# Performance work log

Hardware: AMD Instinct MI355X
Metric: run time of the kernel (lower is better)

Reference implementation:

```python
import jax, jax.numpy as jnp
import numpy as np

HEAD_DIM = 64
NUM_HEADS = 32
ROPE_THETA = 10000.0


def _rope_cos_sin(seq_len, dim, theta, dtype):
    inv_freq = 1.0 / (theta ** (jnp.arange(0, dim, 2, dtype=jnp.float32) / dim))
    t = jnp.arange(seq_len, dtype=jnp.float32)
    freqs = jnp.outer(t, inv_freq)  # [T, dim/2]
    return jnp.cos(freqs).astype(dtype), jnp.sin(freqs).astype(dtype)


def _apply_rope(x, cos, sin):
    # x: [B, T, H, D]; GPT-NeoX style (split halves), matching flash-attn rotary (interleaved=False)
    d2 = x.shape[-1] // 2
    x1, x2 = x[..., :d2], x[..., d2:]
    c = cos[None, :, None, :]
    s = sin[None, :, None, :]
    return jnp.concatenate([x1 * c - x2 * s, x2 * c + x1 * s], axis=-1)


def setup_inputs() -> dict:
    key = jax.random.key(0)
    ks = jax.random.split(key, 8)
    B, T, Dm = 2, 2048, 2048
    H, Dh = NUM_HEADS, HEAD_DIM
    sc = 1.0 / np.sqrt(Dm)
    return {
        "hidden_states": jax.random.normal(ks[0], (B, T, Dm), jnp.float32),
        "v1": jax.random.normal(ks[1], (B, T, H, Dh), jnp.float32),
        "lambda1": jax.random.uniform(ks[2], (), jnp.float32),
        "Wq": jax.random.normal(ks[3], (Dm, Dm), jnp.float32) * sc,
        "Wk": jax.random.normal(ks[4], (Dm, Dm), jnp.float32) * sc,
        "Wv": jax.random.normal(ks[5], (Dm, Dm), jnp.float32) * sc,
        "Wo": jax.random.normal(ks[6], (Dm, Dm), jnp.float32) * sc,
        "lambda2": jnp.float32(0.5),
    }


def reference(hidden_states, v1, lambda1, Wq, Wk, Wv, Wo, lambda2):
    B, T, Dm = hidden_states.shape
    H, Dh = NUM_HEADS, HEAD_DIM
    # QKV projections + head split
    q = (hidden_states @ Wq).reshape(B, T, H, Dh)
    k = (hidden_states @ Wk).reshape(B, T, H, Dh)
    v = (hidden_states @ Wv).reshape(B, T, H, Dh)
    # Value residual mixing: V' = lambda1 * V_1 + lambda2 * V_n
    v = lambda1 * v1 + lambda2 * v
    # RoPE (seqlen_offset = 0, no cache)
    cos, sin = _rope_cos_sin(T, Dh, ROPE_THETA, q.dtype)
    q = _apply_rope(q, cos, sin)
    k = _apply_rope(k, cos, sin)
    # Causal attention (flash_attn_func(..., causal=True) equivalent)
    scale = 1.0 / np.sqrt(Dh)
    scores = jnp.einsum("bqhd,bkhd->bhqk", q, k) * scale
    causal = jnp.tril(jnp.ones((T, T), dtype=bool))
    scores = jnp.where(causal[None, None], scores, jnp.finfo(scores.dtype).min)
    probs = jax.nn.softmax(scores, axis=-1)
    o = jnp.einsum("bhqk,bkhd->bqhd", probs, v).reshape(B, T, Dm)
    return o @ Wo
```

## Files before the change

kernel.cpp:

```cpp
#include <hip/hip_runtime.h>
#include <hip/hip_bf16.h>
#include <math.h>

typedef __bf16 bf16;
typedef __bf16 bf16x8 __attribute__((ext_vector_type(8)));
typedef __bf16 bf16x4 __attribute__((ext_vector_type(4)));
typedef float  f32x4  __attribute__((ext_vector_type(4)));
typedef short  sv4    __attribute__((ext_vector_type(4)));

#define B_  2
#define T_  2048
#define DM  2048
#define H_  32
#define DH  64

__device__ __forceinline__ bf16x8 load8(const bf16* p) {
    return *reinterpret_cast<const bf16x8*>(p);
}

__device__ __forceinline__ void gld16(const bf16* g, bf16* l) {
    __builtin_amdgcn_global_load_lds(
        (const __attribute__((address_space(1))) unsigned int*)g,
        (__attribute__((address_space(3))) unsigned int*)l, 16, 0, 0);
}

__global__ void k_convert(const float* __restrict__ in, bf16* __restrict__ out, int n4) {
    int i = blockIdx.x * blockDim.x + threadIdx.x;
    if (i < n4) {
        float4 v = reinterpret_cast<const float4*>(in)[i];
        bf16x4 o;
        o[0] = (bf16)v.x; o[1] = (bf16)v.y; o[2] = (bf16)v.z; o[3] = (bf16)v.w;
        reinterpret_cast<bf16x4*>(out)[i] = o;
    }
}

__global__ void k_transposeW(const float* __restrict__ Wq, const float* __restrict__ Wk,
                             const float* __restrict__ Wv, const float* __restrict__ Wo,
                             bf16* __restrict__ WqT, bf16* __restrict__ WkT,
                             bf16* __restrict__ WvT, bf16* __restrict__ WoT) {
    const float* in; bf16* out;
    switch (blockIdx.z) {
        case 0: in = Wq; out = WqT; break;
        case 1: in = Wk; out = WkT; break;
        case 2: in = Wv; out = WvT; break;
        default: in = Wo; out = WoT; break;
    }
    __shared__ float tile[32][33];
    int tx = threadIdx.x, ty = threadIdx.y;
    int x0 = blockIdx.x * 32, y0 = blockIdx.y * 32;
    #pragma unroll
    for (int i = 0; i < 4; i++)
        tile[ty + i*8][tx] = in[(size_t)(y0 + ty + i*8) * DM + x0 + tx];
    __syncthreads();
    #pragma unroll
    for (int i = 0; i < 4; i++)
        out[(size_t)(x0 + ty + i*8) * DM + y0 + tx] = (bf16)tile[tx][ty + i*8];
}

template<int OUT_BF16>
__global__ __launch_bounds__(256)
void k_gemm(const bf16* __restrict__ A, const bf16* __restrict__ BT,
            void* __restrict__ Cout, int ldc) {
    constexpr int K = 2048;
    __shared__ bf16 ldsA[128 * 32];
    __shared__ bf16 ldsB[128 * 32];
    int tid = threadIdx.x;
    int lane = tid & 63, w = tid >> 6;
    int l16 = lane & 15, quad = lane >> 4;
    int wm = w >> 1, wn = w & 1;
    int mblk = blockIdx.y * 128, nblk = blockIdx.x * 128;

    f32x4 acc[4][4] = {};

    int sgz = ((lane & 3) ^ ((lane >> 3) & 3)) * 8;
    const bf16* gA = A  + (size_t)(mblk + w * 32 + (lane >> 2)) * K + sgz;
    const bf16* gB = BT + (size_t)(nblk + w * 32 + (lane >> 2)) * K + sgz;
    bf16* lA = ldsA + w * 1024;
    bf16* lB = ldsB + w * 1024;
    int sA = (quad ^ ((l16 >> 1) & 3)) * 8;

    for (int k0 = 0; k0 < K; k0 += 32) {
        gld16(gA + k0,          lA);
        gld16(gA + 16 * K + k0, lA + 512);
        gld16(gB + k0,          lB);
        gld16(gB + 16 * K + k0, lB + 512);
        __syncthreads();
        bf16x8 af[4], bfr[4];
        #pragma unroll
        for (int s = 0; s < 4; s++)
            af[s] = *reinterpret_cast<bf16x8*>(&ldsA[(wm * 64 + s * 16 + l16) * 32 + sA]);
        #pragma unroll
        for (int t = 0; t < 4; t++)
            bfr[t] = *reinterpret_cast<bf16x8*>(&ldsB[(wn * 64 + t * 16 + l16) * 32 + sA]);
        #pragma unroll
        for (int s = 0; s < 4; s++)
            #pragma unroll
            for (int t = 0; t < 4; t++)
                acc[s][t] = __builtin_amdgcn_mfma_f32_16x16x32_bf16(af[s], bfr[t], acc[s][t], 0, 0, 0);
        __syncthreads();
    }

    #pragma unroll
    for (int s = 0; s < 4; s++) {
        int row = mblk + wm * 64 + s * 16 + quad * 4;
        #pragma unroll
        for (int t = 0; t < 4; t++) {
            int col = nblk + wn * 64 + t * 16 + l16;
            #pragma unroll
            for (int r = 0; r < 4; r++) {
                if (OUT_BF16)
                    reinterpret_cast<bf16*>(Cout)[(size_t)(row + r) * ldc + col] = (bf16)acc[s][t][r];
                else
                    reinterpret_cast<float*>(Cout)[(size_t)(row + r) * ldc + col] = acc[s][t][r];
            }
        }
    }
}

template<int OUT_BF16>
__global__ __launch_bounds__(512, 2)
void k_gemm256(const bf16* __restrict__ A, const bf16* __restrict__ BT,
               void* __restrict__ Cout, int ldc) {
    constexpr int K = 2048;
    extern __shared__ bf16 lds[];
    const int tid  = threadIdx.x;
    const int lane = tid & 63, w = tid >> 6;
    const int l16  = lane & 15, quad = lane >> 4;
    const int wm   = w >> 2, wn = w & 3;
    const size_t mblk = (size_t)blockIdx.y * 256, nblk = (size_t)blockIdx.x * 256;

    f32x4 acc[8][4] = {};

    const int sg = (((tid & 3) ^ ((tid >> 3) & 3)) << 3);
    const bf16* gA = A  + (mblk + (tid >> 2)) * K + sg;
    const bf16* gB = BT + (nblk + (tid >> 2)) * K + sg;

    const int segr = ((quad ^ ((l16 >> 1) & 3)) << 3);
    const int aoff = (wm * 128 + l16) * 32 + segr;
    const int boff = (wn * 64  + l16) * 32 + segr;

#define STG(kt_, buf_) do { \
    const bf16* ga_ = gA + (kt_) * 32; \
    const bf16* gb_ = gB + (kt_) * 32; \
    bf16* lb_ = lds + (buf_) * 16384 + w * 512; \
    bf16* la_ = lds + (buf_) * 16384 + 8192 + w * 512; \
    gld16(gb_, lb_); gld16(gb_ + 128 * 2048, lb_ + 4096); \
    gld16(ga_, la_); gld16(ga_ + 128 * 2048, la_ + 4096); \
} while (0)

#define BAR  __builtin_amdgcn_s_barrier()
#define PRI1 __builtin_amdgcn_s_setprio(1)
#define PRI0 __builtin_amdgcn_s_setprio(0)
#define VM4  asm volatile("s_waitcnt vmcnt(4)" ::: "memory")
#define VM0  asm volatile("s_waitcnt vmcnt(0)" ::: "memory")

#define TILE(cb_, SG_, VM_) do { \
    const bf16* rb_ = lds + (cb_) + boff; \
    const bf16* ra_ = lds + (cb_) + 8192 + aoff; \
    bf16x8 af[8], bq[4]; \
    _Pragma("unroll") for (int i_ = 0; i_ < 8; ++i_) \
        af[i_] = *reinterpret_cast<const bf16x8*>(ra_ + i_ * 512); \
    _Pragma("unroll") for (int i_ = 0; i_ < 4; ++i_) \
        bq[i_] = *reinterpret_cast<const bf16x8*>(rb_ + i_ * 512); \
    SG_; \
    VM_; \
    BAR; \
    PRI1; \
    _Pragma("unroll") for (int mi_ = 0; mi_ < 8; ++mi_) \
        _Pragma("unroll") for (int ni_ = 0; ni_ < 4; ++ni_) \
            acc[mi_][ni_] = __builtin_amdgcn_mfma_f32_16x16x32_bf16( \
                af[mi_], bq[ni_], acc[mi_][ni_], 0, 0, 0); \
    PRI0; \
} while (0)

    STG(0, 0); STG(1, 1);
    VM4;
    BAR;

    #pragma unroll 1
    for (int t = 0; t < 60; t += 3) {
        TILE(0,     STG(t + 2, 2), VM4);
        TILE(16384, STG(t + 3, 0), VM4);
        TILE(32768, STG(t + 4, 1), VM4);
    }
    TILE(0,     STG(62, 2), VM4);
    TILE(16384, STG(63, 0), VM4);
    TILE(32768, (void)0,    VM0);
    TILE(0,     (void)0,    (void)0);

#undef STG
#undef BAR
#undef PRI1
#undef PRI0
#undef VM4
#undef VM0
#undef TILE

    #pragma unroll
    for (int mt = 0; mt < 8; ++mt) {
        size_t row = mblk + wm * 128 + mt * 16 + quad * 4;
        #pragma unroll
        for (int nt = 0; nt < 4; ++nt) {
            size_t col = nblk + wn * 64 + nt * 16 + l16;
            #pragma unroll
            for (int r = 0; r < 4; ++r) {
                if (OUT_BF16)
                    reinterpret_cast<bf16*>(Cout)[(row + r) * (size_t)ldc + col] = (bf16)acc[mt][nt][r];
                else
                    reinterpret_cast<float*>(Cout)[(row + r) * (size_t)ldc + col] = acc[mt][nt][r];
            }
        }
    }
}

namespace {
struct GemmLdsInit {
    GemmLdsInit() {
        (void)hipFuncSetAttribute(
            reinterpret_cast<const void*>(&k_gemm256<1>),
            hipFuncAttributeMaxDynamicSharedMemorySize, 98304);
    }
};
GemmLdsInit g_ldsInit;
}

__global__ void k_tab(float2* __restrict__ tab) {
    int id = blockIdx.x * 256 + threadIdx.x;
    int i = id & 31, t = id >> 5;
    float inv = __builtin_amdgcn_exp2f(-(float)i * 0.41524101186092037f);
    float ang = (float)t * inv;
    float s, c;
    __sincosf(ang, &s, &c);
    tab[id] = make_float2(c, s);
}

__global__ void k_rope(bf16* __restrict__ qkv, const float2* __restrict__ tab) {
    int id = blockIdx.x * 256 + threadIdx.x;
    int j   = id & 3;
    int h   = (id >> 2) & 31;
    int sel = (id >> 7) & 1;
    int t   = (id >> 8) & 2047;
    int b   = id >> 19;
    size_t base = ((size_t)(b * T_ + t)) * 6144 + sel * 2048 + h * 64 + j * 8;
    bf16x8 x1 = load8(qkv + base);
    bf16x8 x2 = load8(qkv + base + 32);
    const float2* tp = tab + t * 32 + j * 8;
    bf16x8 o1, o2;
    #pragma unroll
    for (int e = 0; e < 8; e++) {
        float c = tp[e].x, s = tp[e].y;
        float a = (float)x1[e], v = (float)x2[e];
        o1[e] = (bf16)(a * c - v * s);
        o2[e] = (bf16)(v * c + a * s);
    }
    *reinterpret_cast<bf16x8*>(qkv + base)      = o1;
    *reinterpret_cast<bf16x8*>(qkv + base + 32) = o2;
}

__global__ void k_combinev(const float* __restrict__ v1, const bf16* __restrict__ qkv,
                           const float* __restrict__ l1p, const float* __restrict__ l2p,
                           bf16* __restrict__ vT) {
    __shared__ float tile[64 * 33];
    float l1 = l1p[0], l2 = l2p[0];
    int b = blockIdx.y >> 5, h = blockIdx.y & 31;
    int t0 = blockIdx.x * 32;
    int tid = threadIdx.x;
    int d = tid & 63, tr = tid >> 6;
    #pragma unroll
    for (int i = 0; i < 8; i++) {
        int t = t0 + i * 4 + tr;
        size_t iv1 = ((size_t)(b * T_ + t)) * 2048 + h * 64 + d;
        size_t ivg = ((size_t)(b * T_ + t)) * 6144 + 4096 + h * 64 + d;
        tile[d * 33 + i * 4 + tr] = l1 * v1[iv1] + l2 * (float)qkv[ivg];
    }
    __syncthreads();
    int tl = tid & 31, dr = tid >> 5;
    #pragma unroll
    for (int j = 0; j < 8; j++) {
        int d2 = dr + j * 8;
        vT[((size_t)((b * H_ + h) * 64 + d2)) * T_ + t0 + tl] = (bf16)tile[d2 * 33 + tl];
    }
}

__global__ __launch_bounds__(256)
void k_attn(const bf16* __restrict__ qkv, const bf16* __restrict__ vT, bf16* __restrict__ o) {
    __shared__ bf16 ldsK[64 * 64];
    __shared__ bf16 ldsV[64 * 64];
    int bx = blockIdx.x;
    int bh = blockIdx.y;
    int b = bh >> 5, h = bh & 31;
    int tid = threadIdx.x;
    int lane = tid & 63, w = tid >> 6;
    int l16 = lane & 15, quad = lane >> 4;

    int rl = lane >> 3, sg = ((lane & 7) ^ rl) * 8;
    const bf16* kgl = qkv + ((size_t)(b * T_) + w * 16 + rl) * 6144 + 2048 + h * 64 + sg;
    const bf16* vgl = vT + ((size_t)bh * DH + w * 16 + rl) * T_ + sg;
    bf16* lKw = ldsK + w * 16 * 64;
    bf16* lVw = ldsV + w * 16 * 64;

    int skey = (quad ^ (l16 & 7)) * 8;
    int skey2 = ((quad + 4) ^ (l16 & 7)) * 8;

    #pragma unroll 1
    for (int pass = 0; pass < 2; pass++) {
        int qt = pass ? (31 - bx) : bx;
        int qbase = qt * 64 + w * 16;

        size_t qrow = (size_t)(b * T_ + qbase + l16) * 6144 + h * 64;
        bf16x8 qf[2];
        #pragma unroll
        for (int half = 0; half < 2; half++) {
            bf16x8 v = load8(qkv + qrow + half * 32 + quad * 8);
            #pragma unroll
            for (int e = 0; e < 8; e++) v[e] = (bf16)((float)v[e] * 0.1803368801f);
            qf[half] = v;
        }

        f32x4 accO[4] = {};
        float m_ = -1e30f, pl = 0.f;

        int nkt = qt + 1;
        for (int kt = 0; kt < nkt; kt++) {
            int key0 = kt * 64;
            #pragma unroll
            for (int j = 0; j < 2; j++) {
                gld16(kgl + (size_t)(key0 + j * 8) * 6144, lKw + j * 512);
                gld16(vgl + (size_t)(j * 8) * T_ + key0,   lVw + j * 512);
            }
            __syncthreads();

            bool diag = (kt == qt);
            f32x4 st[4];
            sv4 pk[4];
            #pragma unroll
            for (int ks = 0; ks < 4; ks++) {
                if (!diag || key0 + ks * 16 <= qbase + 15) {
                    bf16x8 kf0 = *reinterpret_cast<bf16x8*>(&ldsK[(ks * 16 + l16) * 64 + skey]);
                    bf16x8 kf1 = *reinterpret_cast<bf16x8*>(&ldsK[(ks * 16 + l16) * 64 + skey2]);
                    f32x4 z = {};
                    z = __builtin_amdgcn_mfma_f32_16x16x32_bf16(kf0, qf[0], z, 0, 0, 0);
                    z = __builtin_amdgcn_mfma_f32_16x16x32_bf16(kf1, qf[1], z, 0, 0, 0);
                    st[ks] = z;
                } else {
                    st[ks] = (f32x4){-3e38f, -3e38f, -3e38f, -3e38f};
                }
            }

            if (diag) {
                int qcol = qbase + l16;
                #pragma unroll
                for (int ks = 0; ks < 4; ks++)
                    #pragma unroll
                    for (int r = 0; r < 4; r++)
                        if (key0 + ks * 16 + quad * 4 + r > qcol) st[ks][r] = -3e38f;
            }

            float mx = st[0][0];
            #pragma unroll
            for (int ks = 0; ks < 4; ks++)
                #pragma unroll
                for (int r = 0; r < 4; r++) mx = fmaxf(mx, st[ks][r]);
            mx = fmaxf(mx, __shfl_xor(mx, 16));
            mx = fmaxf(mx, __shfl_xor(mx, 32));
            if (__any(mx > m_)) {
                float nm = fmaxf(m_, mx);
                float alpha = __builtin_amdgcn_exp2f(m_ - nm);
                m_ = nm;
                pl *= alpha;
                #pragma unroll
                for (int n2 = 0; n2 < 4; n2++) accO[n2] *= alpha;
            }
            float rsum = 0.f;
            #pragma unroll
            for (int ks = 0; ks < 4; ks++) {
                bf16x4 ph;
                #pragma unroll
                for (int r = 0; r < 4; r++) {
                    float p = __builtin_amdgcn_exp2f(st[ks][r] - m_);
                    rsum += p;
                    ph[r] = (bf16)p;
                }
                pk[ks] = __builtin_bit_cast(sv4, ph);
            }
            pl += rsum;

            #pragma unroll
            for (int ks = 0; ks < 4; ks++) {
                if (!diag || key0 + ks * 16 <= qbase + 15) {
                    int svf = ((ks * 2 + (quad >> 1)) ^ (l16 & 7)) * 8 + (quad & 1) * 4;
                    #pragma unroll
                    for (int n2 = 0; n2 < 4; n2++) {
                        sv4 vf = *reinterpret_cast<sv4*>(&ldsV[(n2 * 16 + l16) * 64 + svf]);
                        accO[n2] = __builtin_amdgcn_mfma_f32_16x16x16bf16_1k(
                            vf, pk[ks], accO[n2], 0, 0, 0);
                    }
                }
            }
            __syncthreads();
        }

        float l = pl;
        l += __shfl_xor(l, 16);
        l += __shfl_xor(l, 32);
        float inv = 1.0f / l;
        int query = qbase + l16;
        #pragma unroll
        for (int n2 = 0; n2 < 4; n2++) {
            bf16x4 ov;
            #pragma unroll
            for (int r = 0; r < 4; r++) ov[r] = (bf16)(accO[n2][r] * inv);
            *reinterpret_cast<bf16x4*>(
                &o[(size_t)(b * T_ + query) * DM + h * 64 + n2 * 16 + quad * 4]) = ov;
        }
    }
}

extern "C" void kernel_launch(void* const* d_in, const int* in_sizes, int n_in,
                              void* d_out, int out_size, void* d_ws, size_t ws_size,
                              hipStream_t stream) {
    const float* hs   = (const float*)d_in[0];
    const float* v1   = (const float*)d_in[1];
    const float* lam1 = (const float*)d_in[2];
    const float* Wq   = (const float*)d_in[3];
    const float* Wk   = (const float*)d_in[4];
    const float* Wv   = (const float*)d_in[5];
    const float* Wo   = (const float*)d_in[6];
    const float* lam2 = (const float*)d_in[7];

    char* ws = (char*)d_ws;
    bf16* hs_bf = (bf16*)(ws);
    float2* tab = (float2*)(ws);
    bf16* Wcat  = (bf16*)(ws + 16777216);
    bf16* WoT   = (bf16*)(ws + 41943040);
    bf16* qkv   = (bf16*)(ws + 50331648);
    bf16* vT_bf = (bf16*)(ws + 100663296);
    bf16* o_bf  = (bf16*)(ws + 117440512);

    k_convert<<<8192, 256, 0, stream>>>(hs, hs_bf, 2097152);
    k_transposeW<<<dim3(64, 64, 4), dim3(32, 8), 0, stream>>>(
        Wq, Wk, Wv, Wo, Wcat, Wcat + 4194304, Wcat + 8388608, WoT);

    k_gemm256<1><<<dim3(24, 16), 512, 98304, stream>>>(hs_bf, Wcat, (void*)qkv, 6144);

    k_tab<<<256, 256, 0, stream>>>(tab);
    k_rope<<<4096, 256, 0, stream>>>(qkv, tab);

    k_combinev<<<dim3(64, 64), 256, 0, stream>>>(v1, qkv, lam1, lam2, vT_bf);

    k_attn<<<dim3(16, 64), 256, 0, stream>>>(qkv, vT_bf, o_bf);

    k_gemm<0><<<dim3(16, 32), 256, 0, stream>>>(o_bf, WoT, d_out, 2048);
}
```

Baseline: 430.3 us.

## Restructure QKV GEMM with K=64 double-buffered tiles and interleaved MFMA/LDS schedule

The 256x256 QKV GEMM moves from K=32 triple-buffered LDS stages to K=64 double-buffered stages (128 KB LDS). Each tile is split into four MFMA sub-phases with LDS fragment loads and global-to-LDS stages interleaved between barriers, and the LDS swizzle is widened to 8 segments. Block indices are also remapped with a 1D grid so blocks are assigned in an XCD-aware order. This aims to halve barrier and loop overhead per K step and to overlap memory traffic with compute. The cost is more barriers per tile, and the larger LDS footprint likely rules out two blocks per CU.

```diff
diff --git a/kernel.cpp b/kernel.cpp
--- a/kernel.cpp
+++ b/kernel.cpp
@@ -127,71 +127,90 @@
     const int lane = tid & 63, w = tid >> 6;
     const int l16  = lane & 15, quad = lane >> 4;
     const int wm   = w >> 2, wn = w & 3;
-    const size_t mblk = (size_t)blockIdx.y * 256, nblk = (size_t)blockIdx.x * 256;
+    const int nb   = (blockIdx.x & 7) * 48 + (blockIdx.x >> 3);
+    const size_t mblk = (size_t)(nb / 24) * 256, nblk = (size_t)(nb % 24) * 256;
 
     f32x4 acc[8][4] = {};
 
-    const int sg = (((tid & 3) ^ ((tid >> 3) & 3)) << 3);
-    const bf16* gA = A  + (mblk + (tid >> 2)) * K + sg;
-    const bf16* gB = BT + (nblk + (tid >> 2)) * K + sg;
-
-    const int segr = ((quad ^ ((l16 >> 1) & 3)) << 3);
-    const int aoff = (wm * 128 + l16) * 32 + segr;
-    const int boff = (wn * 64  + l16) * 32 + segr;
-
-#define STG(kt_, buf_) do { \
-    const bf16* ga_ = gA + (kt_) * 32; \
-    const bf16* gb_ = gB + (kt_) * 32; \
-    bf16* lb_ = lds + (buf_) * 16384 + w * 512; \
-    bf16* la_ = lds + (buf_) * 16384 + 8192 + w * 512; \
-    gld16(gb_, lb_); gld16(gb_ + 128 * 2048, lb_ + 4096); \
-    gld16(ga_, la_); gld16(ga_ + 128 * 2048, la_ + 4096); \
+    const int lsg = (((tid & 7) ^ ((tid >> 3) & 7)) << 3);
+    const bf16* gA = A  + (mblk + (tid >> 3)) * K + lsg;
+    const bf16* gB = BT + (nblk + (tid >> 3)) * K + lsg;
+    bf16* lw = lds + w * 512;
+
+    const int seg0 = ((quad ^ (l16 & 7)) << 3);
+    const int seg1 = (((4 + quad) ^ (l16 & 7)) << 3);
+
+#define STG(kt_, r_) do { \
+    const bf16* g_ = (((r_) & 2) ? gA : gB) + (size_t)(((r_) & 1) << 7) * K + (kt_) * 64; \
+    bf16* l_ = lw + (((kt_) & 1) << 15) + ((r_) << 13); \
+    gld16(g_, l_); gld16(g_ + (size_t)64 * K, l_ + 4096); \
 } while (0)
 
+#define LDA(cb_, mh_) do { \
+    _Pragma("unroll") for (int i_ = 0; i_ < 4; ++i_) { \
+        int ro_ = (cb_) + 16384 + (wm * 128 + ((mh_) * 4 + i_) * 16 + l16) * 64; \
+        av[i_][0] = *reinterpret_cast<const bf16x8*>(lds + ro_ + seg0); \
+        av[i_][1] = *reinterpret_cast<const bf16x8*>(lds + ro_ + seg1); \
+    } \
+} while (0)
+
+#define LDB(cb_, nh_) do { \
+    _Pragma("unroll") for (int j_ = 0; j_ < 2; ++j_) { \
+        int ni_ = (nh_) * 2 + j_; \
+        int ro_ = (cb_) + (wn * 64 + ni_ * 16 + l16) * 64; \
+        bv[ni_][0] = *reinterpret_cast<const bf16x8*>(lds + ro_ + seg0); \
+        bv[ni_][1] = *reinterpret_cast<const bf16x8*>(lds + ro_ + seg1); \
+    } \
+} while (0)
+
+#define MF(mh_, nh_) do { \
+    __builtin_amdgcn_s_setprio(1); \
+    _Pragma("unroll") for (int i_ = 0; i_ < 4; ++i_) \
+        _Pragma("unroll") for (int j_ = 0; j_ < 2; ++j_) { \
+            int mi_ = (mh_) * 4 + i_, ni_ = (nh_) * 2 + j_; \
+            acc[mi_][ni_] = __builtin_amdgcn_mfma_f32_16x16x32_bf16( \
+                av[i_][0], bv[ni_][0], acc[mi_][ni_], 0, 0, 0); \
+            acc[mi_][ni_] = __builtin_amdgcn_mfma_f32_16x16x32_bf16( \
+                av[i_][1], bv[ni_][1], acc[mi_][ni_], 0, 0, 0); \
+        } \
+    __builtin_amdgcn_s_setprio(0); \
+} while (0)
+
 #define BAR  __builtin_amdgcn_s_barrier()
-#define PRI1 __builtin_amdgcn_s_setprio(1)
-#define PRI0 __builtin_amdgcn_s_setprio(0)
+#define LGK0 asm volatile("s_waitcnt lgkmcnt(0)" ::: "memory")
 #define VM4  asm volatile("s_waitcnt vmcnt(4)" ::: "memory")
 #define VM0  asm volatile("s_waitcnt vmcnt(0)" ::: "memory")
 
-#define TILE(cb_, SG_, VM_) do { \
-    const bf16* rb_ = lds + (cb_) + boff; \
-    const bf16* ra_ = lds + (cb_) + 8192 + aoff; \
-    bf16x8 af[8], bq[4]; \
-    _Pragma("unroll") for (int i_ = 0; i_ < 8; ++i_) \
-        af[i_] = *reinterpret_cast<const bf16x8*>(ra_ + i_ * 512); \
-    _Pragma("unroll") for (int i_ = 0; i_ < 4; ++i_) \
-        bq[i_] = *reinterpret_cast<const bf16x8*>(rb_ + i_ * 512); \
-    SG_; \
-    VM_; \
-    BAR; \
-    PRI1; \
-    _Pragma("unroll") for (int mi_ = 0; mi_ < 8; ++mi_) \
-        _Pragma("unroll") for (int ni_ = 0; ni_ < 4; ++ni_) \
-            acc[mi_][ni_] = __builtin_amdgcn_mfma_f32_16x16x32_bf16( \
-                af[mi_], bq[ni_], acc[mi_][ni_], 0, 0, 0); \
-    PRI0; \
+#define TILE(cb_, S1_, S3_, S4_, VM_) do { \
+    bf16x8 av[4][2], bv[4][2]; \
+    LDA(cb_, 0); LDB(cb_, 0); \
+    S1_; BAR; LGK0; MF(0, 0); BAR; \
+    LDB(cb_, 1); \
+    BAR; LGK0; MF(0, 1); BAR; \
+    LDA(cb_, 1); \
+    S3_; BAR; LGK0; MF(1, 0); BAR; \
+    S4_; BAR; MF(1, 1); VM_; BAR; \
 } while (0)
 
-    STG(0, 0); STG(1, 1);
+    STG(0, 0); STG(0, 1); STG(0, 2); STG(0, 3);
+    STG(1, 0); STG(1, 1);
     VM4;
     BAR;
 
     #pragma unroll 1
-    for (int t = 0; t < 60; t += 3) {
-        TILE(0,     STG(t + 2, 2), VM4);
-        TILE(16384, STG(t + 3, 0), VM4);
-        TILE(32768, STG(t + 4, 1), VM4);
-    }
-    TILE(0,     STG(62, 2), VM4);
-    TILE(16384, STG(63, 0), VM4);
-    TILE(32768, (void)0,    VM0);
-    TILE(0,     (void)0,    (void)0);
+    for (int t = 0; t < 30; t += 2) {
+        TILE(0,     { STG(t + 1, 2); STG(t + 1, 3); }, STG(t + 2, 0), STG(t + 2, 1), VM4);
+        TILE(32768, { STG(t + 2, 2); STG(t + 2, 3); }, STG(t + 3, 0), STG(t + 3, 1), VM4);
+    }
+    TILE(0,     { STG(31, 2); STG(31, 3); }, (void)0, (void)0, VM0);
+    TILE(32768, (void)0, (void)0, (void)0, (void)0);
 
 #undef STG
+#undef LDA
+#undef LDB
+#undef MF
 #undef BAR
-#undef PRI1
-#undef PRI0
+#undef LGK0
 #undef VM4
 #undef VM0
 #undef TILE
@@ -218,7 +237,7 @@
     GemmLdsInit() {
         (void)hipFuncSetAttribute(
             reinterpret_cast<const void*>(&k_gemm256<1>),
-            hipFuncAttributeMaxDynamicSharedMemorySize, 98304);
+            hipFuncAttributeMaxDynamicSharedMemorySize, 131072);
     }
 };
 GemmLdsInit g_ldsInit;
@@ -441,7 +460,7 @@
     k_transposeW<<<dim3(64, 64, 4), dim3(32, 8), 0, stream>>>(
         Wq, Wk, Wv, Wo, Wcat, Wcat + 4194304, Wcat + 8388608, WoT);
 
-    k_gemm256<1><<<dim3(24, 16), 512, 98304, stream>>>(hs_bf, Wcat, (void*)qkv, 6144);
+    k_gemm256<1><<<384, 512, 131072, stream>>>(hs_bf, Wcat, (void*)qkv, 6144);
 
     k_tab<<<256, 256, 0, stream>>>(tab);
     k_rope<<<4096, 256, 0, stream>>>(qkv, tab);
```

After: 433.5 us. About the same (+0.7%).
